# Kernel tuning notes

Hardware: AMD Instinct MI355X
Metric: run time of the kernel (lower is better)

Reference implementation:

```python
import jax, jax.numpy as jnp
import numpy as np

B, S, D, H = 1, 2048, 1024, 16
HD = D // H
FF = 4 * D
EPS_LN = 1e-5
EPS_ATTN = 1e-6


def _layernorm(x, g, b):
    mu = jnp.mean(x, axis=-1, keepdims=True)
    var = jnp.mean(jnp.square(x - mu), axis=-1, keepdims=True)
    return (x - mu) * jax.lax.rsqrt(var + EPS_LN) * g + b


def setup_inputs() -> dict:
    key = jax.random.key(0)
    ks = jax.random.split(key, 12)
    w = lambda k, shape: (jax.random.normal(k, shape, jnp.float32) * 0.02)
    return {
        "x": jax.random.normal(ks[0], (B, S, D), jnp.float32),
        "Wq": w(ks[1], (D, D)), "bq": jnp.zeros((D,), jnp.float32),
        "Wk": w(ks[2], (D, D)), "bk": jnp.zeros((D,), jnp.float32),
        "Wv": w(ks[3], (D, D)), "bv": jnp.zeros((D,), jnp.float32),
        "Wo": w(ks[4], (D, D)), "bo": jnp.zeros((D,), jnp.float32),
        "W1": w(ks[5], (FF, D)), "bb1": jnp.zeros((FF,), jnp.float32),
        "W2": w(ks[6], (D, FF)), "bb2": jnp.zeros((D,), jnp.float32),
        "g1": jnp.ones((D,), jnp.float32), "be1": jnp.zeros((D,), jnp.float32),
        "g2": jnp.ones((D,), jnp.float32), "be2": jnp.zeros((D,), jnp.float32),
    }


def reference(x, Wq, bq, Wk, bk, Wv, bv, Wo, bo, W1, bb1, W2, bb2, g1, be1, g2, be2):
    # --- pre-norm causal linear attention ---
    h = _layernorm(x, g1, be1)                     # (B,S,D)
    def heads(t):
        return t.reshape(B, S, H, HD).transpose(0, 2, 1, 3)  # (B,H,S,hd)
    q = heads(h @ Wq.T + bq)
    k = heads(h @ Wk.T + bk)
    v = heads(h @ Wv.T + bv)
    # feature map phi(x) = elu(x) + 1 (strictly positive)
    q = jax.nn.elu(q) + 1.0
    k = jax.nn.elu(k) + 1.0
    # causal cumulative state: S_t = sum_{i<=t} k_i v_i^T ; z_t = sum_{i<=t} k_i
    kv = jnp.cumsum(jnp.einsum("bhsd,bhse->bhsde", k, v), axis=2)  # (B,H,S,hd,hd)
    z = jnp.cumsum(k, axis=2)                                       # (B,H,S,hd)
    num = jnp.einsum("bhsd,bhsde->bhse", q, kv)                    # (B,H,S,hd)
    den = jnp.einsum("bhsd,bhsd->bhs", q, z) + EPS_ATTN
    attn = (num / den[..., None]).transpose(0, 2, 1, 3).reshape(B, S, D)
    attn = attn @ Wo.T + bo
    x = x + attn
    # --- FFN (GELU exact, matching torch nn.GELU default) ---
    h2 = _layernorm(x, g2, be2)
    ff = jax.nn.gelu(h2 @ W1.T + bb1, approximate=False) @ W2.T + bb2
    return x + ff
```

## Files before the change

kernel.cpp:

```cpp
#include <hip/hip_runtime.h>
#include <hip/hip_bf16.h>
#include <math.h>

constexpr int S  = 2048;
constexpr int D  = 1024;
constexpr int H  = 16;
constexpr int HD = 64;
constexpr int FF = 4096;
constexpr int NC  = 32;
constexpr int CHK = 64;
constexpr int QS  = 3 * D;

typedef __attribute__((ext_vector_type(8))) short bf16x8;
typedef __attribute__((ext_vector_type(4))) float f32x4;

__device__ inline unsigned short f2bf(float f) {
    unsigned int u = __float_as_uint(f);
    u = (u + 0x7FFFu + ((u >> 16) & 1u)) >> 16;
    return (unsigned short)u;
}

constexpr int DD4 = D * D / 4;
constexpr int FD4 = FF * D / 4;
constexpr int CVT_TOTAL4 = 4 * DD4 + 2 * FD4;

__global__ __launch_bounds__(256) void cvt6(const float* __restrict__ Wq,
                                            const float* __restrict__ Wk,
                                            const float* __restrict__ Wv,
                                            const float* __restrict__ Wo,
                                            const float* __restrict__ W1,
                                            const float* __restrict__ W2,
                                            unsigned short* __restrict__ Wqkvb,
                                            unsigned short* __restrict__ Wob,
                                            unsigned short* __restrict__ W1b,
                                            unsigned short* __restrict__ W2b) {
    int i = blockIdx.x * 256 + threadIdx.x;
    if (i >= CVT_TOTAL4) return;
    const float* s;
    unsigned short* dp;
    if (i < DD4)                 { s = Wq + (size_t)i * 4;               dp = Wqkvb + (size_t)i * 4; }
    else if (i < 2 * DD4)        { s = Wk + (size_t)(i - DD4) * 4;       dp = Wqkvb + (size_t)i * 4; }
    else if (i < 3 * DD4)        { s = Wv + (size_t)(i - 2 * DD4) * 4;   dp = Wqkvb + (size_t)i * 4; }
    else if (i < 4 * DD4)        { s = Wo + (size_t)(i - 3 * DD4) * 4;   dp = Wob + (size_t)(i - 3 * DD4) * 4; }
    else if (i < 4 * DD4 + FD4)  { s = W1 + (size_t)(i - 4 * DD4) * 4;   dp = W1b + (size_t)(i - 4 * DD4) * 4; }
    else                         { s = W2 + (size_t)(i - 4 * DD4 - FD4) * 4; dp = W2b + (size_t)(i - 4 * DD4 - FD4) * 4; }
    float4 v = *(const float4*)s;
    ushort4 o = { f2bf(v.x), f2bf(v.y), f2bf(v.z), f2bf(v.w) };
    *(ushort4*)dp = o;
}

__global__ __launch_bounds__(256) void layernorm_bf16(const float* __restrict__ x,
                                                      const float* __restrict__ g,
                                                      const float* __restrict__ b,
                                                      unsigned short* __restrict__ out) {
    const int row = blockIdx.x, tid = threadIdx.x;
    float4 v = ((const float4*)(x + (size_t)row * D))[tid];
    float s  = v.x + v.y + v.z + v.w;
    float ss = v.x*v.x + v.y*v.y + v.z*v.z + v.w*v.w;
    #pragma unroll
    for (int off = 32; off > 0; off >>= 1) {
        s  += __shfl_down(s, off);
        ss += __shfl_down(ss, off);
    }
    __shared__ float sw[4], ssw[4];
    if ((tid & 63) == 0) { sw[tid >> 6] = s; ssw[tid >> 6] = ss; }
    __syncthreads();
    s  = sw[0] + sw[1] + sw[2] + sw[3];
    ss = ssw[0] + ssw[1] + ssw[2] + ssw[3];
    const float mu = s * (1.0f / D);
    const float rs = rsqrtf(ss * (1.0f / D) - mu * mu + 1e-5f);
    float4 gv = ((const float4*)g)[tid];
    float4 bv = ((const float4*)b)[tid];
    ushort4 o = { f2bf((v.x - mu) * rs * gv.x + bv.x),
                  f2bf((v.y - mu) * rs * gv.y + bv.y),
                  f2bf((v.z - mu) * rs * gv.z + bv.z),
                  f2bf((v.w - mu) * rs * gv.w + bv.w) };
    ((ushort4*)(out + (size_t)row * D))[tid] = o;
}

template <int KS>
__global__ __launch_bounds__(256) void reduce_ln(const float* __restrict__ part,
                                                 const float* __restrict__ bias,
                                                 const float* __restrict__ res,
                                                 float* __restrict__ x2,
                                                 const float* __restrict__ g,
                                                 const float* __restrict__ b,
                                                 unsigned short* __restrict__ out) {
    const int row = blockIdx.x, tid = threadIdx.x;
    const size_t i4 = (size_t)row * 256 + tid;
    float4 a = ((const float4*)part)[i4];
    #pragma unroll
    for (int z = 1; z < KS; ++z) {
        float4 p = ((const float4*)part)[(size_t)z * S * 256 + i4];
        a.x += p.x; a.y += p.y; a.z += p.z; a.w += p.w;
    }
    float4 bi = ((const float4*)bias)[tid];
    float4 r  = ((const float4*)res)[i4];
    a.x += bi.x + r.x; a.y += bi.y + r.y; a.z += bi.z + r.z; a.w += bi.w + r.w;
    ((float4*)x2)[i4] = a;
    float s  = a.x + a.y + a.z + a.w;
    float ss = a.x*a.x + a.y*a.y + a.z*a.z + a.w*a.w;
    #pragma unroll
    for (int off = 32; off > 0; off >>= 1) {
        s  += __shfl_down(s, off);
        ss += __shfl_down(ss, off);
    }
    __shared__ float sw[4], ssw[4];
    if ((tid & 63) == 0) { sw[tid >> 6] = s; ssw[tid >> 6] = ss; }
    __syncthreads();
    s  = sw[0] + sw[1] + sw[2] + sw[3];
    ss = ssw[0] + ssw[1] + ssw[2] + ssw[3];
    const float mu = s * (1.0f / D);
    const float rs = rsqrtf(ss * (1.0f / D) - mu * mu + 1e-5f);
    float4 gv = ((const float4*)g)[tid];
    float4 bv = ((const float4*)b)[tid];
    ushort4 o = { f2bf((a.x - mu) * rs * gv.x + bv.x),
                  f2bf((a.y - mu) * rs * gv.y + bv.y),
                  f2bf((a.z - mu) * rs * gv.z + bv.z),
                  f2bf((a.w - mu) * rs * gv.w + bv.w) };
    ((ushort4*)(out + (size_t)row * D))[tid] = o;
}

template <int KS>
__global__ __launch_bounds__(256) void reduce_bias_res(const float* __restrict__ part,
                                                       const float* __restrict__ bias,
                                                       const float* __restrict__ res,
                                                       float* __restrict__ out,
                                                       int N4, int total4) {
    int i = blockIdx.x * 256 + threadIdx.x;
    if (i >= total4) return;
    float4 a = ((const float4*)part)[i];
    #pragma unroll
    for (int z = 1; z < KS; ++z) {
        float4 p = ((const float4*)part)[(size_t)z * total4 + i];
        a.x += p.x; a.y += p.y; a.z += p.z; a.w += p.w;
    }
    float4 b = ((const float4*)bias)[i % N4];
    float4 r = ((const float4*)res)[i];
    a.x += b.x + r.x; a.y += b.y + r.y; a.z += b.z + r.z; a.w += b.w + r.w;
    ((float4*)out)[i] = a;
}

enum { EPI_F32 = 0, EPI_QKV = 1, EPI_GELU_BF16 = 2, EPI_PART = 3 };

template <int EPI>
__global__ __launch_bounds__(512, 4) void gemm_bt(const unsigned short* __restrict__ A,
                                                  const unsigned short* __restrict__ W,
                                                  const float* __restrict__ bias,
                                                  const float* __restrict__ bias2,
                                                  const float* __restrict__ bias3,
                                                  void* __restrict__ outp,
                                                  int M, int N, int K, int kSplit) {
    __shared__ unsigned short As[128 * 32];
    __shared__ unsigned short Bs[128 * 32];
    const int tid  = threadIdx.x;
    const int tileM = blockIdx.x * 128;
    const int tileN = blockIdx.y * 128;
    const int w    = tid >> 6, lane = tid & 63;
    const int wm   = (w >> 2) * 64, wn = (w & 3) * 32;
    const int lr   = lane & 15, lk = lane >> 4;
    const int kLen   = K / kSplit;
    const int kStart = blockIdx.z * kLen;
    const int kEnd   = kStart + kLen;
    const int srow = tid >> 2, skc = (tid & 3) * 8;

    f32x4 acc[4][2];
    #pragma unroll
    for (int i = 0; i < 4; ++i)
        #pragma unroll
        for (int j = 0; j < 2; ++j) acc[i][j] = (f32x4)(0.0f);

    for (int k0 = kStart; k0 < kEnd; k0 += 32) {
        __builtin_amdgcn_global_load_lds(
            (const __attribute__((address_space(1))) unsigned int*)
                (A + (size_t)(tileM + srow) * K + k0 + skc),
            (__attribute__((address_space(3))) unsigned int*)&As[tid * 8],
            16, 0, 0);
        __builtin_amdgcn_global_load_lds(
            (const __attribute__((address_space(1))) unsigned int*)
                (W + (size_t)(tileN + srow) * K + k0 + skc),
            (__attribute__((address_space(3))) unsigned int*)&Bs[tid * 8],
            16, 0, 0);
        __syncthreads();
        bf16x8 af[4], bfv[2];
        #pragma unroll
        for (int i = 0; i < 4; ++i)
            af[i]  = *(const bf16x8*)&As[(wm + i * 16 + lr) * 32 + lk * 8];
        #pragma unroll
        for (int j = 0; j < 2; ++j)
            bfv[j] = *(const bf16x8*)&Bs[(wn + j * 16 + lr) * 32 + lk * 8];
        #pragma unroll
        for (int i = 0; i < 4; ++i)
            #pragma unroll
            for (int j = 0; j < 2; ++j)
                acc[i][j] = __builtin_amdgcn_mfma_f32_16x16x32_bf16(af[i], bfv[j], acc[i][j], 0, 0, 0);
        __syncthreads();
    }

    #pragma unroll
    for (int i = 0; i < 4; ++i) {
        const int rbase = tileM + wm + i * 16 + lk * 4;
        #pragma unroll
        for (int j = 0; j < 2; ++j) {
            const int col = tileN + wn + j * 16 + lr;
            #pragma unroll
            for (int r = 0; r < 4; ++r) {
                const int row = rbase + r;
                const size_t off = (size_t)row * N + col;
                float v = acc[i][j][r];
                if constexpr (EPI == EPI_PART) {
                    ((float*)outp)[(size_t)blockIdx.z * (size_t)M * (size_t)N + off] = v;
                } else if constexpr (EPI == EPI_QKV) {
                    float bc = (col < D) ? bias[col] : ((col < 2 * D) ? bias2[col - D] : bias3[col - 2 * D]);
                    v += bc;
                    if (col < 2 * D) v = v > 0.0f ? v + 1.0f : __expf(v);
                    ((float*)outp)[off] = v;
                } else if constexpr (EPI == EPI_GELU_BF16) {
                    v += bias[col];
                    float gl = 0.5f * v * (1.0f + erff(v * 0.70710678118654752f));
                    ((unsigned short*)outp)[off] = f2bf(gl);
                } else {
                    v += bias[col];
                    ((float*)outp)[off] = v;
                }
            }
        }
    }
}

__global__ __launch_bounds__(256) void attn_chunk_sums(const float* __restrict__ qkv,
                                                       float* __restrict__ KVc,
                                                       float* __restrict__ Zc) {
    const int c = blockIdx.x, h = blockIdx.y, tid = threadIdx.x;
    __shared__ float Kc[CHK * HD], Vc[CHK * HD];
    const int s0 = c * CHK;
    #pragma unroll
    for (int p = 0; p < 4; ++p) {
        int cc = p * 256 + tid;
        int t = cc >> 4, dp = (cc & 15) * 4;
        *(float4*)&Kc[t * HD + dp] = *(const float4*)(qkv + (size_t)(s0 + t) * QS + D     + h * HD + dp);
        *(float4*)&Vc[t * HD + dp] = *(const float4*)(qkv + (size_t)(s0 + t) * QS + 2 * D + h * HD + dp);
    }
    __syncthreads();
    const int d = tid >> 2, e0 = (tid & 3) * 16;
    float acc[16];
    #pragma unroll
    for (int j = 0; j < 16; ++j) acc[j] = 0.0f;
    float zacc = 0.0f;
    for (int t = 0; t < CHK; ++t) {
        float kv = Kc[t * HD + d];
        zacc += kv;
        #pragma unroll
        for (int j = 0; j < 16; ++j) acc[j] += kv * Vc[t * HD + e0 + j];
    }
    float* op = KVc + ((size_t)(h * NC + c) * HD + d) * HD + e0;
    #pragma unroll
    for (int j = 0; j < 16; ++j) op[j] = acc[j];
    if ((tid & 3) == 0) Zc[(size_t)(h * NC + c) * HD + d] = zacc;
}

__global__ __launch_bounds__(256) void attn_prefix(float* __restrict__ KVc,
                                                   float* __restrict__ Zc) {
    const int h = blockIdx.y;
    const int elem = blockIdx.x * 256 + threadIdx.x;
    size_t base = (size_t)h * NC * (HD * HD) + elem;
    float run = 0.0f;
    for (int c = 0; c < NC; ++c) {
        float t = KVc[base + (size_t)c * (HD * HD)];
        KVc[base + (size_t)c * (HD * HD)] = run;
        run += t;
    }
    if (blockIdx.x == 0 && threadIdx.x < HD) {
        size_t zb = (size_t)h * NC * HD + threadIdx.x;
        float zr = 0.0f;
        for (int c = 0; c < NC; ++c) {
            float t = Zc[zb + (size_t)c * HD];
            Zc[zb + (size_t)c * HD] = zr;
            zr += t;
        }
    }
}

__global__ __launch_bounds__(256) void attn_out(const float* __restrict__ qkv,
                                                const float* __restrict__ KVpre,
                                                const float* __restrict__ Zpre,
                                                unsigned short* __restrict__ attn) {
    const int c = blockIdx.x, h = blockIdx.y, tid = threadIdx.x;
    __shared__ float Qc[CHK * HD], KVs[CHK * HD], Pre[HD * HD], Sc[CHK * CHK];
    __shared__ float zp[HD], den[CHK];
    const int s0 = c * CHK;
    #pragma unroll
    for (int p = 0; p < 4; ++p) {
        int cc = p * 256 + tid;
        int t = cc >> 4, dp = (cc & 15) * 4;
        *(float4*)&Qc[t * HD + dp]  = *(const float4*)(qkv + (size_t)(s0 + t) * QS +     h * HD + dp);
        *(float4*)&KVs[t * HD + dp] = *(const float4*)(qkv + (size_t)(s0 + t) * QS + D + h * HD + dp);
        ((float4*)Pre)[cc] = *(const float4*)(KVpre + (size_t)(h * NC + c) * (HD * HD) + cc * 4);
    }
    if (tid < HD) zp[tid] = Zpre[(size_t)(h * NC + c) * HD + tid];
    __syncthreads();

    const int tt = tid >> 2, i0 = (tid & 3) * 16;
    for (int i = i0; i < i0 + 16; ++i) {
        float sv = 0.0f;
        for (int d2 = 0; d2 < HD; ++d2) sv += Qc[tt * HD + d2] * KVs[i * HD + d2];
        Sc[tt * CHK + i] = (i <= tt) ? sv : 0.0f;
    }
    __syncthreads();

    if (tid < CHK) {
        float dv = 1e-6f;
        for (int d2 = 0; d2 < HD; ++d2) dv += Qc[tid * HD + d2] * zp[d2];
        for (int i = 0; i < CHK; ++i) dv += Sc[tid * CHK + i];
        den[tid] = dv;
    }
    #pragma unroll
    for (int p = 0; p < 4; ++p) {
        int cc = p * 256 + tid;
        int t = cc >> 4, dp = (cc & 15) * 4;
        *(float4*)&KVs[t * HD + dp] = *(const float4*)(qkv + (size_t)(s0 + t) * QS + 2 * D + h * HD + dp);
    }
    __syncthreads();

    float o[16];
    #pragma unroll
    for (int j = 0; j < 16; ++j) o[j] = 0.0f;
    for (int d2 = 0; d2 < HD; ++d2) {
        float qv = Qc[tt * HD + d2];
        float sv = Sc[tt * CHK + d2];
        #pragma unroll
        for (int j = 0; j < 16; ++j)
            o[j] += qv * Pre[d2 * HD + i0 + j] + sv * KVs[d2 * HD + i0 + j];
    }
    const float inv = 1.0f / den[tt];
    unsigned short* op = attn + (size_t)(s0 + tt) * D + h * HD + i0;
    #pragma unroll
    for (int j0 = 0; j0 < 16; j0 += 4) {
        ushort4 ov = { f2bf(o[j0] * inv), f2bf(o[j0 + 1] * inv),
                       f2bf(o[j0 + 2] * inv), f2bf(o[j0 + 3] * inv) };
        *(ushort4*)(op + j0) = ov;
    }
}

extern "C" void kernel_launch(void* const* d_in, const int* in_sizes, int n_in,
                              void* d_out, int out_size, void* d_ws, size_t ws_size,
                              hipStream_t stream) {
    const float* x   = (const float*)d_in[0];
    const float* Wq  = (const float*)d_in[1];
    const float* bq  = (const float*)d_in[2];
    const float* Wk  = (const float*)d_in[3];
    const float* bk  = (const float*)d_in[4];
    const float* Wv  = (const float*)d_in[5];
    const float* bv  = (const float*)d_in[6];
    const float* Wo  = (const float*)d_in[7];
    const float* bo  = (const float*)d_in[8];
    const float* W1  = (const float*)d_in[9];
    const float* b1  = (const float*)d_in[10];
    const float* W2  = (const float*)d_in[11];
    const float* b2  = (const float*)d_in[12];
    const float* g1  = (const float*)d_in[13];
    const float* be1 = (const float*)d_in[14];
    const float* g2  = (const float*)d_in[15];
    const float* be2 = (const float*)d_in[16];
    float* out = (float*)d_out;

    char* wsp = (char*)d_ws;
    auto alloc = [&](size_t bytes) {
        char* p = wsp;
        wsp += (bytes + 255) & ~(size_t)255;
        return p;
    };
    unsigned short* h1   = (unsigned short*)alloc((size_t)S * D * 2);
    unsigned short* attn = (unsigned short*)alloc((size_t)S * D * 2);
    unsigned short* gbuf = (unsigned short*)alloc((size_t)S * FF * 2);
    float* x2   = (float*)alloc((size_t)S * D * 4);
    unsigned short* Wqkvb = (unsigned short*)alloc((size_t)3 * D * D * 2);
    unsigned short* Wob   = (unsigned short*)alloc((size_t)D * D * 2);
    unsigned short* W1b   = (unsigned short*)alloc((size_t)FF * D * 2);
    unsigned short* W2b   = (unsigned short*)alloc((size_t)D * FF * 2);
    float* KVc  = (float*)alloc((size_t)H * NC * HD * HD * 4);
    float* Zc   = (float*)alloc((size_t)H * NC * HD * 4);
    char* uni = (char*)alloc((size_t)32 * 1024 * 1024);
    float* qkv   = (float*)uni;
    float* parts = (float*)uni;

    cvt6<<<(CVT_TOTAL4 + 255) / 256, 256, 0, stream>>>(Wq, Wk, Wv, Wo, W1, W2,
                                                       Wqkvb, Wob, W1b, W2b);

    layernorm_bf16<<<S, 256, 0, stream>>>(x, g1, be1, h1);

    gemm_bt<EPI_QKV><<<dim3(S / 128, 3 * D / 128, 1), 512, 0, stream>>>(
        h1, Wqkvb, bq, bk, bv, qkv, S, 3 * D, D, 1);

    attn_chunk_sums<<<dim3(NC, H), 256, 0, stream>>>(qkv, KVc, Zc);
    attn_prefix<<<dim3(16, H), 256, 0, stream>>>(KVc, Zc);
    attn_out<<<dim3(NC, H), 256, 0, stream>>>(qkv, KVc, Zc, attn);

    gemm_bt<EPI_PART><<<dim3(S / 128, D / 128, 2), 512, 0, stream>>>(
        attn, Wob, nullptr, nullptr, nullptr, parts, S, D, D, 2);
    reduce_ln<2><<<S, 256, 0, stream>>>(parts, bo, x, x2, g2, be2, h1);

    gemm_bt<EPI_GELU_BF16><<<dim3(S / 128, FF / 128, 1), 512, 0, stream>>>(
        h1, W1b, b1, nullptr, nullptr, gbuf, S, FF, D, 1);

    gemm_bt<EPI_PART><<<dim3(S / 128, D / 128, 4), 512, 0, stream>>>(
        gbuf, W2b, nullptr, nullptr, nullptr, parts, S, D, FF, 4);
    reduce_bias_res<4><<<(S * D / 4 + 255) / 256, 256, 0, stream>>>(
        parts, b2, x2, out, D / 4, S * D / 4);
}
```

Baseline: 291.6 us.

## Double-buffer GEMM LDS tiles with BK=64, XOR swizzle, and 4 waves per block

Restructures the bf16 GEMM to use double-buffered shared-memory tiles with K-step 64. The next tile's global-to-LDS loads are issued before computing the current one, and there is one barrier per iteration instead of two. An XOR swizzle is added to avoid LDS bank conflicts. Blocks drop to 256 threads, with each wave computing a 64x64 sub-tile (4x4 MFMAs) for more register reuse. The Wo projection's split-K rises from 2 to 4 to keep enough blocks. The cost is higher LDS use per block (64KB) and lower occupancy, plus more partial-sum traffic for the Wo reduction.

After: 280.3 us. 1.04x faster.

```diff
diff --git a/kernel.cpp b/kernel.cpp
--- a/kernel.cpp
+++ b/kernel.cpp
@@ -144,64 +144,84 @@
 enum { EPI_F32 = 0, EPI_QKV = 1, EPI_GELU_BF16 = 2, EPI_PART = 3 };
 
 template <int EPI>
-__global__ __launch_bounds__(512, 4) void gemm_bt(const unsigned short* __restrict__ A,
+__global__ __launch_bounds__(256, 2) void gemm_bt(const unsigned short* __restrict__ A,
                                                   const unsigned short* __restrict__ W,
                                                   const float* __restrict__ bias,
                                                   const float* __restrict__ bias2,
                                                   const float* __restrict__ bias3,
                                                   void* __restrict__ outp,
                                                   int M, int N, int K, int kSplit) {
-    __shared__ unsigned short As[128 * 32];
-    __shared__ unsigned short Bs[128 * 32];
+    __shared__ unsigned short As[2][128 * 64];
+    __shared__ unsigned short Bs[2][128 * 64];
     const int tid  = threadIdx.x;
     const int tileM = blockIdx.x * 128;
     const int tileN = blockIdx.y * 128;
     const int w    = tid >> 6, lane = tid & 63;
-    const int wm   = (w >> 2) * 64, wn = (w & 3) * 32;
+    const int wm   = (w >> 1) * 64, wn = (w & 1) * 64;
     const int lr   = lane & 15, lk = lane >> 4;
+    const int sw   = (lr >> 1) & 7;
     const int kLen   = K / kSplit;
     const int kStart = blockIdx.z * kLen;
     const int kEnd   = kStart + kLen;
-    const int srow = tid >> 2, skc = (tid & 3) * 8;
-
-    f32x4 acc[4][2];
+
+    f32x4 acc[4][4];
     #pragma unroll
     for (int i = 0; i < 4; ++i)
         #pragma unroll
-        for (int j = 0; j < 2; ++j) acc[i][j] = (f32x4)(0.0f);
-
-    for (int k0 = kStart; k0 < kEnd; k0 += 32) {
-        __builtin_amdgcn_global_load_lds(
-            (const __attribute__((address_space(1))) unsigned int*)
-                (A + (size_t)(tileM + srow) * K + k0 + skc),
-            (__attribute__((address_space(3))) unsigned int*)&As[tid * 8],
-            16, 0, 0);
-        __builtin_amdgcn_global_load_lds(
-            (const __attribute__((address_space(1))) unsigned int*)
-                (W + (size_t)(tileN + srow) * K + k0 + skc),
-            (__attribute__((address_space(3))) unsigned int*)&Bs[tid * 8],
-            16, 0, 0);
+        for (int j = 0; j < 4; ++j) acc[i][j] = (f32x4)(0.0f);
+
+    auto stage = [&](int buf, int k0) {
+        #pragma unroll
+        for (int p = 0; p < 4; ++p) {
+            const int c   = p * 256 + tid;
+            const int row = c >> 3;
+            const int kc  = (c & 7) ^ ((row >> 1) & 7);
+            __builtin_amdgcn_global_load_lds(
+                (const __attribute__((address_space(1))) unsigned int*)
+                    (A + (size_t)(tileM + row) * K + k0 + kc * 8),
+                (__attribute__((address_space(3))) unsigned int*)&As[buf][c * 8],
+                16, 0, 0);
+            __builtin_amdgcn_global_load_lds(
+                (const __attribute__((address_space(1))) unsigned int*)
+                    (W + (size_t)(tileN + row) * K + k0 + kc * 8),
+                (__attribute__((address_space(3))) unsigned int*)&Bs[buf][c * 8],
+                16, 0, 0);
+        }
+    };
+
+    stage(0, kStart);
+    __syncthreads();
+    int buf = 0;
+    for (int k0 = kStart; k0 < kEnd; k0 += 64) {
+        if (k0 + 64 < kEnd) stage(buf ^ 1, k0 + 64);
+        #pragma unroll
+        for (int kk = 0; kk < 2; ++kk) {
+            bf16x8 af[4], bfv[4];
+            #pragma unroll
+            for (int i = 0; i < 4; ++i) {
+                const int row = wm + i * 16 + lr;
+                af[i] = *(const bf16x8*)&As[buf][row * 64 + ((((kk << 2) | lk) ^ sw) << 3)];
+            }
+            #pragma unroll
+            for (int j = 0; j < 4; ++j) {
+                const int row = wn + j * 16 + lr;
+                bfv[j] = *(const bf16x8*)&Bs[buf][row * 64 + ((((kk << 2) | lk) ^ sw) << 3)];
+            }
+            #pragma unroll
+            for (int i = 0; i < 4; ++i)
+                #pragma unroll
+                for (int j = 0; j < 4; ++j)
+                    acc[i][j] = __builtin_amdgcn_mfma_f32_16x16x32_bf16(af[i], bfv[j], acc[i][j], 0, 0, 0);
+        }
         __syncthreads();
-        bf16x8 af[4], bfv[2];
-        #pragma unroll
-        for (int i = 0; i < 4; ++i)
-            af[i]  = *(const bf16x8*)&As[(wm + i * 16 + lr) * 32 + lk * 8];
-        #pragma unroll
-        for (int j = 0; j < 2; ++j)
-            bfv[j] = *(const bf16x8*)&Bs[(wn + j * 16 + lr) * 32 + lk * 8];
-        #pragma unroll
-        for (int i = 0; i < 4; ++i)
-            #pragma unroll
-            for (int j = 0; j < 2; ++j)
-                acc[i][j] = __builtin_amdgcn_mfma_f32_16x16x32_bf16(af[i], bfv[j], acc[i][j], 0, 0, 0);
-        __syncthreads();
+        buf ^= 1;
     }
 
     #pragma unroll
     for (int i = 0; i < 4; ++i) {
         const int rbase = tileM + wm + i * 16 + lk * 4;
         #pragma unroll
-        for (int j = 0; j < 2; ++j) {
+        for (int j = 0; j < 4; ++j) {
             const int col = tileN + wn + j * 16 + lr;
             #pragma unroll
             for (int r = 0; r < 4; ++r) {
@@ -389,21 +409,21 @@
 
     layernorm_bf16<<<S, 256, 0, stream>>>(x, g1, be1, h1);
 
-    gemm_bt<EPI_QKV><<<dim3(S / 128, 3 * D / 128, 1), 512, 0, stream>>>(
+    gemm_bt<EPI_QKV><<<dim3(S / 128, 3 * D / 128, 1), 256, 0, stream>>>(
         h1, Wqkvb, bq, bk, bv, qkv, S, 3 * D, D, 1);
 
     attn_chunk_sums<<<dim3(NC, H), 256, 0, stream>>>(qkv, KVc, Zc);
     attn_prefix<<<dim3(16, H), 256, 0, stream>>>(KVc, Zc);
     attn_out<<<dim3(NC, H), 256, 0, stream>>>(qkv, KVc, Zc, attn);
 
-    gemm_bt<EPI_PART><<<dim3(S / 128, D / 128, 2), 512, 0, stream>>>(
-        attn, Wob, nullptr, nullptr, nullptr, parts, S, D, D, 2);
-    reduce_ln<2><<<S, 256, 0, stream>>>(parts, bo, x, x2, g2, be2, h1);
-
-    gemm_bt<EPI_GELU_BF16><<<dim3(S / 128, FF / 128, 1), 512, 0, stream>>>(
+    gemm_bt<EPI_PART><<<dim3(S / 128, D / 128, 4), 256, 0, stream>>>(
+        attn, Wob, nullptr, nullptr, nullptr, parts, S, D, D, 4);
+    reduce_ln<4><<<S, 256, 0, stream>>>(parts, bo, x, x2, g2, be2, h1);
+
+    gemm_bt<EPI_GELU_BF16><<<dim3(S / 128, FF / 128, 1), 256, 0, stream>>>(
         h1, W1b, b1, nullptr, nullptr, gbuf, S, FF, D, 1);
 
-    gemm_bt<EPI_PART><<<dim3(S / 128, D / 128, 4), 512, 0, stream>>>(
+    gemm_bt<EPI_PART><<<dim3(S / 128, D / 128, 4), 256, 0, stream>>>(
         gbuf, W2b, nullptr, nullptr, nullptr, parts, S, D, FF, 4);
     reduce_bias_res<4><<<(S * D / 4 + 255) / 256, 256, 0, stream>>>(
         parts, b2, x2, out, D / 4, S * D / 4);
```
